# Performance work log

Hardware: AMD Instinct MI355X
Metric: run time of the kernel (lower is better)

The kernel has to match this reference:

```python
import jax, jax.numpy as jnp
import numpy as np

B, H, S, D = 2, 16, 2048, 64
NUM_BUCKETS = 32
MAX_DISTANCE = 256


def setup_inputs() -> dict:
    key = jax.random.key(0)
    kq, kk, kv, kb, kl = jax.random.split(key, 5)
    q = jax.random.normal(kq, (B, H, S, D), dtype=jnp.float32)
    k = jax.random.normal(kk, (B, H, S, D), dtype=jnp.float32)
    v = jax.random.normal(kv, (B, H, S, D), dtype=jnp.float32)
    bias_table = jax.random.normal(kb, (NUM_BUCKETS, H), dtype=jnp.float32)
    event_length = jax.random.randint(kl, (B,), 1, S + 1, dtype=jnp.int64)
    return {"q": q, "k": k, "v": v, "bias_table": bias_table, "event_length": event_length}


def _relative_position_bucket(relative_position):
    # T5-style bucketing exactly as the torch module: n = -rel_pos
    half = NUM_BUCKETS // 2  # 16
    n = -relative_position
    is_small = n < half
    # guard log for the branch not taken (n<=0); where() masks it out
    nf = jnp.maximum(n, 1).astype(jnp.float32)
    val_if_large = half + jnp.minimum(
        jnp.log(nf / half) / np.log(MAX_DISTANCE / half) * (NUM_BUCKETS - half),
        NUM_BUCKETS - 1 - half,
    ).astype(jnp.int32)
    ret = jnp.where(is_small, n, val_if_large)
    return jnp.clip(ret, 0, NUM_BUCKETS - 1)


def _compute_bias(bias_table, seq_len):
    ctx = jnp.arange(seq_len)[:, None]
    mem = jnp.arange(seq_len)[None, :]
    rp_bucket = _relative_position_bucket(mem - ctx)  # (S,S)
    values = bias_table[rp_bucket]                    # (S,S,H)
    return jnp.transpose(values, (2, 0, 1))[None]     # (1,H,S,S)


def reference(q, k, v, bias_table, event_length):
    seq_len = q.shape[2]
    head_dim = q.shape[3]
    # scaled QK^T: (B,H,S,S)
    logits = jnp.einsum("bhsd,bhtd->bhst", q, k) / np.sqrt(head_dim).astype(np.float32)
    logits = logits + _compute_bias(bias_table, seq_len)
    # key-side padding mask from per-event lengths
    mask = jnp.arange(seq_len)[None, None, None, :] < event_length[:, None, None, None]
    logits = jnp.where(mask, logits, jnp.float32(-1e9))
    attn = jax.nn.softmax(logits, axis=-1)
    # dropout p=0.01 omitted (eval-mode deterministic reference)
    return jnp.einsum("bhst,bhtd->bhsd", attn, v)
```

## Files before the change

kernel.cpp:

```cpp
#include <hip/hip_runtime.h>
#include <hip/hip_bf16.h>

#define B_ 2
#define H_ 16
#define S_ 2048
#define D_ 64
#define BQ 128
#define BK 64
#define LDSTR 72
#define LOG2E 1.4426950408889634f
#define FIXM 10.0f

#if __has_builtin(__builtin_amdgcn_exp2f)
#define EXP2F(x) __builtin_amdgcn_exp2f(x)
#else
#define EXP2F(x) __expf((x) * 0.6931471805599453f)
#endif

typedef _Float16 half8 __attribute__((ext_vector_type(8)));
typedef _Float16 half4 __attribute__((ext_vector_type(4)));
typedef __fp16   fp16x2 __attribute__((ext_vector_type(2)));
typedef float floatx4 __attribute__((ext_vector_type(4)));

__global__ __launch_bounds__(256, 2)
void t5_attn_kernel(const float* __restrict__ qg_, const float* __restrict__ kg_,
                    const float* __restrict__ vg_, const float* __restrict__ bt,
                    const int* __restrict__ elen, float* __restrict__ outg_)
{
    __shared__ __align__(16) _Float16 Kl[2][BK][LDSTR];
    __shared__ __align__(16) _Float16 Vt[2][D_][LDSTR];
    __shared__ __align__(16) _Float16 Pl[4][32][LDSTR];
    __shared__ float lut[256];

    const int qblk = blockIdx.x;
    const int h    = blockIdx.y;
    const int b    = blockIdx.z;
    const int tid  = threadIdx.x;
    const int wave = tid >> 6;
    const int lane = tid & 63;
    const int quad = lane >> 4;
    const int t16  = lane & 15;

    {
        int n = tid;
        int bucket;
        if (n < 16) {
            bucket = n;
        } else {
            int vl = (int)(__log2f((float)n * 0.0625f) * 4.0f);
            bucket = 16 + (vl < 15 ? vl : 15);
        }
        lut[n] = bt[bucket * H_ + h] * LOG2E - FIXM;
    }
    const float sh_next = FIXM - bt[h] * LOG2E;
    const float sh_far  = FIXM - bt[31 * H_ + h] * LOG2E;

    const int len = (elen[1] == 0) ? elen[2 * b] : elen[b];
    const int ntiles = (len + BK - 1) >> 6;

    const size_t bh = ((size_t)b * H_ + h) * (size_t)(S_ * D_);
    const float* qg = qg_ + bh;
    const float* kg = kg_ + bh;
    const float* vg = vg_ + bh;
    float*       og = outg_ + bh;

    half8 qf[2][2];
    #pragma unroll
    for (int rg = 0; rg < 2; ++rg) {
        const float qscale = 0.125f * LOG2E;
        const int row = qblk * BQ + wave * 32 + rg * 16 + t16;
        const float* qp = qg + (size_t)row * D_ + quad * 8;
        #pragma unroll
        for (int c = 0; c < 2; ++c) {
            const float4* p = reinterpret_cast<const float4*>(qp + c * 32);
            float4 x0 = p[0], x1 = p[1];
            half8 hv;
            hv[0] = (_Float16)(x0.x * qscale); hv[1] = (_Float16)(x0.y * qscale);
            hv[2] = (_Float16)(x0.z * qscale); hv[3] = (_Float16)(x0.w * qscale);
            hv[4] = (_Float16)(x1.x * qscale); hv[5] = (_Float16)(x1.y * qscale);
            hv[6] = (_Float16)(x1.z * qscale); hv[7] = (_Float16)(x1.w * qscale);
            qf[rg][c] = hv;
        }
    }

    floatx4 zero4 = {0.f, 0.f, 0.f, 0.f};
    floatx4 acc[2][4];
    float l_[2];
    #pragma unroll
    for (int rg = 0; rg < 2; ++rg) {
        #pragma unroll
        for (int nb = 0; nb < 4; ++nb) acc[rg][nb] = zero4;
        l_[rg] = 0.f;
    }

    const int i_lo = qblk * BQ + wave * 32;

    float4 kx[2][2];
    float  vx[16];
    auto prefetch = [&](int kt) {
        #pragma unroll
        for (int it = 0; it < 2; ++it) {
            int idx = tid + it * 256;
            int row = idx >> 3;
            int c8  = (idx & 7) << 3;
            const float4* p = reinterpret_cast<const float4*>(
                kg + ((size_t)(kt * BK + row) * D_ + c8));
            kx[it][0] = p[0];
            kx[it][1] = p[1];
        }
        #pragma unroll
        for (int it = 0; it < 2; ++it) {
            int key8 = kt * BK + wave * 8 + it * 32;
            #pragma unroll
            for (int jj = 0; jj < 8; ++jj)
                vx[it * 8 + jj] = vg[(size_t)(key8 + jj) * D_ + lane];
        }
    };
    auto stage = [&](int buf) {
        #pragma unroll
        for (int it = 0; it < 2; ++it) {
            int idx = tid + it * 256;
            int row = idx >> 3;
            int c8  = (idx & 7) << 3;
            float4 x0 = kx[it][0], x1 = kx[it][1];
            half8 hv;
            hv[0]=(_Float16)x0.x; hv[1]=(_Float16)x0.y; hv[2]=(_Float16)x0.z; hv[3]=(_Float16)x0.w;
            hv[4]=(_Float16)x1.x; hv[5]=(_Float16)x1.y; hv[6]=(_Float16)x1.z; hv[7]=(_Float16)x1.w;
            *reinterpret_cast<half8*>(&Kl[buf][row][c8]) = hv;
        }
        #pragma unroll
        for (int it = 0; it < 2; ++it) {
            int key8 = wave * 8 + it * 32;
            half8 hv;
            #pragma unroll
            for (int jj = 0; jj < 8; ++jj) hv[jj] = (_Float16)vx[it * 8 + jj];
            *reinterpret_cast<half8*>(&Vt[buf][lane][key8]) = hv;
        }
    };

    prefetch(0);
    stage(0);
    __syncthreads();

    for (int kt = 0; kt < ntiles; ++kt) {
        const int cur = kt & 1;
        const bool more = (kt + 1) < ntiles;
        if (more) prefetch(kt + 1);

        floatx4 sa[2][4];
        #pragma unroll
        for (int rg = 0; rg < 2; ++rg)
            #pragma unroll
            for (int nb = 0; nb < 4; ++nb) sa[rg][nb] = zero4;
        #pragma unroll
        for (int kc = 0; kc < 2; ++kc) {
            #pragma unroll
            for (int nb = 0; nb < 4; ++nb) {
                half8 af = *reinterpret_cast<const half8*>(
                    &Kl[cur][nb * 16 + t16][kc * 32 + quad * 8]);
                sa[0][nb] = __builtin_amdgcn_mfma_f32_16x16x32_f16(af, qf[0][kc], sa[0][nb], 0, 0, 0);
                sa[1][nb] = __builtin_amdgcn_mfma_f32_16x16x32_f16(af, qf[1][kc], sa[1][nb], 0, 0, 0);
            }
        }

        const int base = kt * BK;
        if (i_lo + 31 <= base) {
            #pragma unroll
            for (int rg = 0; rg < 2; ++rg)
                #pragma unroll
                for (int nb = 0; nb < 4; ++nb)
                    #pragma unroll
                    for (int r = 0; r < 4; ++r) sa[rg][nb][r] -= sh_next;
        } else if (i_lo >= base + 279) {
            #pragma unroll
            for (int rg = 0; rg < 2; ++rg)
                #pragma unroll
                for (int nb = 0; nb < 4; ++nb)
                    #pragma unroll
                    for (int r = 0; r < 4; ++r) sa[rg][nb][r] -= sh_far;
        } else {
            #pragma unroll
            for (int rg = 0; rg < 2; ++rg) {
                const int d0 = i_lo + rg * 16 + t16 - base - quad * 4;
                #pragma unroll
                for (int nb = 0; nb < 4; ++nb) {
                    #pragma unroll
                    for (int r = 0; r < 4; ++r) {
                        int d = d0 - nb * 16 - r;
                        d = d < 0 ? 0 : (d > 255 ? 255 : d);
                        sa[rg][nb][r] += lut[d];
                    }
                }
            }
        }
        if ((kt == ntiles - 1) && (len & 63)) {
            #pragma unroll
            for (int nb = 0; nb < 4; ++nb) {
                #pragma unroll
                for (int r = 0; r < 4; ++r) {
                    bool valid = (base + nb * 16 + quad * 4 + r) < len;
                    #pragma unroll
                    for (int rg = 0; rg < 2; ++rg)
                        sa[rg][nb][r] = valid ? sa[rg][nb][r] : -1e30f;
                }
            }
        }

        #pragma unroll
        for (int rg = 0; rg < 2; ++rg) {
            float s = 0.f;
            #pragma unroll
            for (int nb = 0; nb < 4; ++nb)
                #pragma unroll
                for (int r = 0; r < 4; ++r) {
                    sa[rg][nb][r] = EXP2F(sa[rg][nb][r]);
                    s += sa[rg][nb][r];
                }
            l_[rg] += s;
        }

        #pragma unroll
        for (int rg = 0; rg < 2; ++rg) {
            #pragma unroll
            for (int nb = 0; nb < 4; ++nb) {
                fp16x2 lo = __builtin_amdgcn_cvt_pkrtz(sa[rg][nb][0], sa[rg][nb][1]);
                fp16x2 hi = __builtin_amdgcn_cvt_pkrtz(sa[rg][nb][2], sa[rg][nb][3]);
                half4 w;
                w[0] = (_Float16)lo[0]; w[1] = (_Float16)lo[1];
                w[2] = (_Float16)hi[0]; w[3] = (_Float16)hi[1];
                *reinterpret_cast<half4*>(
                    &Pl[wave][rg * 16 + t16][nb * 16 + quad * 4]) = w;
            }
        }
        asm volatile("s_waitcnt lgkmcnt(0)" ::: "memory");

        #pragma unroll
        for (int kc = 0; kc < 2; ++kc) {
            half8 a0 = *reinterpret_cast<const half8*>(
                &Pl[wave][t16][kc * 32 + quad * 8]);
            half8 a1 = *reinterpret_cast<const half8*>(
                &Pl[wave][16 + t16][kc * 32 + quad * 8]);
            #pragma unroll
            for (int nb = 0; nb < 4; ++nb) {
                half8 bv = *reinterpret_cast<const half8*>(
                    &Vt[cur][nb * 16 + t16][kc * 32 + quad * 8]);
                acc[0][nb] = __builtin_amdgcn_mfma_f32_16x16x32_f16(a0, bv, acc[0][nb], 0, 0, 0);
                acc[1][nb] = __builtin_amdgcn_mfma_f32_16x16x32_f16(a1, bv, acc[1][nb], 0, 0, 0);
            }
        }

        if (more) stage(cur ^ 1);
        __syncthreads();
    }

    #pragma unroll
    for (int rg = 0; rg < 2; ++rg) {
        float lv = l_[rg];
        lv += __shfl_xor(lv, 16, 64);
        lv += __shfl_xor(lv, 32, 64);
        float inv = 1.f / lv;
        #pragma unroll
        for (int r = 0; r < 4; ++r) {
            int rowloc = quad * 4 + r;
            float invr = __shfl(inv, (lane & 48) | rowloc, 64);
            const int row = qblk * BQ + wave * 32 + rg * 16 + rowloc;
            #pragma unroll
            for (int nb = 0; nb < 4; ++nb)
                og[(size_t)row * D_ + nb * 16 + t16] = acc[rg][nb][r] * invr;
        }
    }
}

extern "C" void kernel_launch(void* const* d_in, const int* in_sizes, int n_in,
                              void* d_out, int out_size, void* d_ws, size_t ws_size,
                              hipStream_t stream) {
    const float* q  = (const float*)d_in[0];
    const float* k  = (const float*)d_in[1];
    const float* v  = (const float*)d_in[2];
    const float* bt = (const float*)d_in[3];
    const int*   el = (const int*)d_in[4];
    float* out = (float*)d_out;
    dim3 grid(S_ / BQ, H_, B_);
    t5_attn_kernel<<<grid, 256, 0, stream>>>(q, k, v, bt, el, out);
}
```

Baseline: 117.6 us.

## Process key tiles in pairs with register-staged fp16 prefetch and interleaved grid

The key loop now handles two 64-key tiles per iteration. Both K and V tiles are loaded from global memory and converted to fp16 in registers ahead of time, then written to LDS between two barriers, and the P staging buffer is widened to hold 128 keys. This halves the number of loop iterations and barrier points and gives the QK^T MFMAs more independent work. The grid becomes 1D with batch and head interleaved in the low bits, which changes block scheduling order and could balance the uneven per-batch sequence lengths. In exchange it uses more registers and LDS, which may lower occupancy. It also wastes a masked half-pair when the tile count is odd and adds an extra barrier per iteration.

```diff
diff --git a/kernel.cpp b/kernel.cpp
--- a/kernel.cpp
+++ b/kernel.cpp
@@ -8,6 +8,7 @@
 #define BQ 128
 #define BK 64
 #define LDSTR 72
+#define PSTR 136
 #define LOG2E 1.4426950408889634f
 #define FIXM 10.0f
 
@@ -29,12 +30,13 @@
 {
     __shared__ __align__(16) _Float16 Kl[2][BK][LDSTR];
     __shared__ __align__(16) _Float16 Vt[2][D_][LDSTR];
-    __shared__ __align__(16) _Float16 Pl[4][32][LDSTR];
+    __shared__ __align__(16) _Float16 Pl[4][32][PSTR];
     __shared__ float lut[256];
 
-    const int qblk = blockIdx.x;
-    const int h    = blockIdx.y;
-    const int b    = blockIdx.z;
+    const int bx   = blockIdx.x;
+    const int b    = bx & 1;
+    const int h    = (bx >> 1) & 15;
+    const int qblk = bx >> 5;
     const int tid  = threadIdx.x;
     const int wave = tid >> 6;
     const int lane = tid & 63;
@@ -57,6 +59,7 @@
 
     const int len = (elen[1] == 0) ? elen[2 * b] : elen[b];
     const int ntiles = (len + BK - 1) >> 6;
+    const int npairs = (ntiles + 1) >> 1;
 
     const size_t bh = ((size_t)b * H_ + h) * (size_t)(S_ * D_);
     const float* qg = qg_ + bh;
@@ -95,162 +98,188 @@
 
     const int i_lo = qblk * BQ + wave * 32;
 
-    float4 kx[2][2];
-    float  vx[16];
-    auto prefetch = [&](int kt) {
-        #pragma unroll
-        for (int it = 0; it < 2; ++it) {
-            int idx = tid + it * 256;
-            int row = idx >> 3;
-            int c8  = (idx & 7) << 3;
-            const float4* p = reinterpret_cast<const float4*>(
-                kg + ((size_t)(kt * BK + row) * D_ + c8));
-            kx[it][0] = p[0];
-            kx[it][1] = p[1];
-        }
-        #pragma unroll
-        for (int it = 0; it < 2; ++it) {
-            int key8 = kt * BK + wave * 8 + it * 32;
-            #pragma unroll
-            for (int jj = 0; jj < 8; ++jj)
-                vx[it * 8 + jj] = vg[(size_t)(key8 + jj) * D_ + lane];
+    half8 kst[2][2];
+    half8 vst[2][2];
+    const int krow = tid >> 3;
+    const int kc8  = (tid & 7) << 3;
+    auto prefetch = [&](int p) {
+        const int pbase = p * 2 * BK;
+        #pragma unroll
+        for (int t = 0; t < 2; ++t) {
+            #pragma unroll
+            for (int it = 0; it < 2; ++it) {
+                int idx = tid + it * 256;
+                int row = idx >> 3, c8 = (idx & 7) << 3;
+                const float4* pp = reinterpret_cast<const float4*>(
+                    kg + ((size_t)(pbase + t * BK + row) * D_ + c8));
+                float4 x0 = pp[0], x1 = pp[1];
+                half8 hv;
+                hv[0]=(_Float16)x0.x; hv[1]=(_Float16)x0.y; hv[2]=(_Float16)x0.z; hv[3]=(_Float16)x0.w;
+                hv[4]=(_Float16)x1.x; hv[5]=(_Float16)x1.y; hv[6]=(_Float16)x1.z; hv[7]=(_Float16)x1.w;
+                kst[t][it] = hv;
+            }
+            #pragma unroll
+            for (int it = 0; it < 2; ++it) {
+                int key8 = pbase + t * BK + wave * 8 + it * 32;
+                half8 vv;
+                #pragma unroll
+                for (int jj = 0; jj < 8; ++jj)
+                    vv[jj] = (_Float16)vg[(size_t)(key8 + jj) * D_ + lane];
+                vst[t][it] = vv;
+            }
         }
     };
-    auto stage = [&](int buf) {
-        #pragma unroll
-        for (int it = 0; it < 2; ++it) {
-            int idx = tid + it * 256;
-            int row = idx >> 3;
-            int c8  = (idx & 7) << 3;
-            float4 x0 = kx[it][0], x1 = kx[it][1];
-            half8 hv;
-            hv[0]=(_Float16)x0.x; hv[1]=(_Float16)x0.y; hv[2]=(_Float16)x0.z; hv[3]=(_Float16)x0.w;
-            hv[4]=(_Float16)x1.x; hv[5]=(_Float16)x1.y; hv[6]=(_Float16)x1.z; hv[7]=(_Float16)x1.w;
-            *reinterpret_cast<half8*>(&Kl[buf][row][c8]) = hv;
-        }
-        #pragma unroll
-        for (int it = 0; it < 2; ++it) {
-            int key8 = wave * 8 + it * 32;
-            half8 hv;
-            #pragma unroll
-            for (int jj = 0; jj < 8; ++jj) hv[jj] = (_Float16)vx[it * 8 + jj];
-            *reinterpret_cast<half8*>(&Vt[buf][lane][key8]) = hv;
+    auto stage = [&]() {
+        #pragma unroll
+        for (int t = 0; t < 2; ++t) {
+            #pragma unroll
+            for (int it = 0; it < 2; ++it) {
+                int idx = tid + it * 256;
+                int row = idx >> 3, c8 = (idx & 7) << 3;
+                *reinterpret_cast<half8*>(&Kl[t][row][c8]) = kst[t][it];
+                *reinterpret_cast<half8*>(&Vt[t][lane][wave * 8 + it * 32]) = vst[t][it];
+            }
         }
     };
 
     prefetch(0);
-    stage(0);
+    stage();
     __syncthreads();
 
-    for (int kt = 0; kt < ntiles; ++kt) {
-        const int cur = kt & 1;
-        const bool more = (kt + 1) < ntiles;
-        if (more) prefetch(kt + 1);
-
-        floatx4 sa[2][4];
-        #pragma unroll
-        for (int rg = 0; rg < 2; ++rg)
-            #pragma unroll
-            for (int nb = 0; nb < 4; ++nb) sa[rg][nb] = zero4;
+    for (int p = 0; p < npairs; ++p) {
+        const bool more = (p + 1) < npairs;
+
+        floatx4 sa[2][2][4];
+        #pragma unroll
+        for (int t = 0; t < 2; ++t)
+            #pragma unroll
+            for (int rg = 0; rg < 2; ++rg)
+                #pragma unroll
+                for (int nb = 0; nb < 4; ++nb) sa[t][rg][nb] = zero4;
         #pragma unroll
         for (int kc = 0; kc < 2; ++kc) {
             #pragma unroll
             for (int nb = 0; nb < 4; ++nb) {
-                half8 af = *reinterpret_cast<const half8*>(
-                    &Kl[cur][nb * 16 + t16][kc * 32 + quad * 8]);
-                sa[0][nb] = __builtin_amdgcn_mfma_f32_16x16x32_f16(af, qf[0][kc], sa[0][nb], 0, 0, 0);
-                sa[1][nb] = __builtin_amdgcn_mfma_f32_16x16x32_f16(af, qf[1][kc], sa[1][nb], 0, 0, 0);
-            }
-        }
-
-        const int base = kt * BK;
-        if (i_lo + 31 <= base) {
-            #pragma unroll
-            for (int rg = 0; rg < 2; ++rg)
-                #pragma unroll
-                for (int nb = 0; nb < 4; ++nb)
-                    #pragma unroll
-                    for (int r = 0; r < 4; ++r) sa[rg][nb][r] -= sh_next;
-        } else if (i_lo >= base + 279) {
-            #pragma unroll
-            for (int rg = 0; rg < 2; ++rg)
-                #pragma unroll
-                for (int nb = 0; nb < 4; ++nb)
-                    #pragma unroll
-                    for (int r = 0; r < 4; ++r) sa[rg][nb][r] -= sh_far;
-        } else {
-            #pragma unroll
-            for (int rg = 0; rg < 2; ++rg) {
-                const int d0 = i_lo + rg * 16 + t16 - base - quad * 4;
-                #pragma unroll
-                for (int nb = 0; nb < 4; ++nb) {
-                    #pragma unroll
-                    for (int r = 0; r < 4; ++r) {
-                        int d = d0 - nb * 16 - r;
-                        d = d < 0 ? 0 : (d > 255 ? 255 : d);
-                        sa[rg][nb][r] += lut[d];
+                half8 af0 = *reinterpret_cast<const half8*>(
+                    &Kl[0][nb * 16 + t16][kc * 32 + quad * 8]);
+                half8 af1 = *reinterpret_cast<const half8*>(
+                    &Kl[1][nb * 16 + t16][kc * 32 + quad * 8]);
+                sa[0][0][nb] = __builtin_amdgcn_mfma_f32_16x16x32_f16(af0, qf[0][kc], sa[0][0][nb], 0, 0, 0);
+                sa[1][0][nb] = __builtin_amdgcn_mfma_f32_16x16x32_f16(af1, qf[0][kc], sa[1][0][nb], 0, 0, 0);
+                sa[0][1][nb] = __builtin_amdgcn_mfma_f32_16x16x32_f16(af0, qf[1][kc], sa[0][1][nb], 0, 0, 0);
+                sa[1][1][nb] = __builtin_amdgcn_mfma_f32_16x16x32_f16(af1, qf[1][kc], sa[1][1][nb], 0, 0, 0);
+            }
+        }
+
+        if (more) prefetch(p + 1);
+
+        #pragma unroll
+        for (int t = 0; t < 2; ++t) {
+            const int kt = 2 * p + t;
+            const int base = kt * BK;
+            if (kt >= ntiles) {
+                #pragma unroll
+                for (int rg = 0; rg < 2; ++rg)
+                    #pragma unroll
+                    for (int nb = 0; nb < 4; ++nb)
+                        #pragma unroll
+                        for (int r = 0; r < 4; ++r) sa[t][rg][nb][r] = -1e30f;
+            } else if (i_lo + 31 <= base) {
+                #pragma unroll
+                for (int rg = 0; rg < 2; ++rg)
+                    #pragma unroll
+                    for (int nb = 0; nb < 4; ++nb)
+                        #pragma unroll
+                        for (int r = 0; r < 4; ++r) sa[t][rg][nb][r] -= sh_next;
+            } else if (i_lo >= base + 279) {
+                #pragma unroll
+                for (int rg = 0; rg < 2; ++rg)
+                    #pragma unroll
+                    for (int nb = 0; nb < 4; ++nb)
+                        #pragma unroll
+                        for (int r = 0; r < 4; ++r) sa[t][rg][nb][r] -= sh_far;
+            } else {
+                #pragma unroll
+                for (int rg = 0; rg < 2; ++rg) {
+                    const int d0 = i_lo + rg * 16 + t16 - base - quad * 4;
+                    #pragma unroll
+                    for (int nb = 0; nb < 4; ++nb) {
+                        #pragma unroll
+                        for (int r = 0; r < 4; ++r) {
+                            int d = d0 - nb * 16 - r;
+                            d = d < 0 ? 0 : (d > 255 ? 255 : d);
+                            sa[t][rg][nb][r] += lut[d];
+                        }
                     }
                 }
             }
-        }
-        if ((kt == ntiles - 1) && (len & 63)) {
-            #pragma unroll
-            for (int nb = 0; nb < 4; ++nb) {
-                #pragma unroll
-                for (int r = 0; r < 4; ++r) {
-                    bool valid = (base + nb * 16 + quad * 4 + r) < len;
-                    #pragma unroll
-                    for (int rg = 0; rg < 2; ++rg)
-                        sa[rg][nb][r] = valid ? sa[rg][nb][r] : -1e30f;
+            if ((kt == ntiles - 1) && (len & 63)) {
+                #pragma unroll
+                for (int nb = 0; nb < 4; ++nb) {
+                    #pragma unroll
+                    for (int r = 0; r < 4; ++r) {
+                        bool valid = (base + nb * 16 + quad * 4 + r) < len;
+                        #pragma unroll
+                        for (int rg = 0; rg < 2; ++rg)
+                            sa[t][rg][nb][r] = valid ? sa[t][rg][nb][r] : -1e30f;
+                    }
                 }
             }
-        }
-
-        #pragma unroll
-        for (int rg = 0; rg < 2; ++rg) {
-            float s = 0.f;
-            #pragma unroll
-            for (int nb = 0; nb < 4; ++nb)
-                #pragma unroll
-                for (int r = 0; r < 4; ++r) {
-                    sa[rg][nb][r] = EXP2F(sa[rg][nb][r]);
-                    s += sa[rg][nb][r];
+            #pragma unroll
+            for (int rg = 0; rg < 2; ++rg) {
+                float s = 0.f;
+                #pragma unroll
+                for (int nb = 0; nb < 4; ++nb)
+                    #pragma unroll
+                    for (int r = 0; r < 4; ++r) {
+                        sa[t][rg][nb][r] = EXP2F(sa[t][rg][nb][r]);
+                        s += sa[t][rg][nb][r];
+                    }
+                l_[rg] += s;
+            }
+        }
+
+        #pragma unroll
+        for (int t = 0; t < 2; ++t) {
+            #pragma unroll
+            for (int rg = 0; rg < 2; ++rg) {
+                #pragma unroll
+                for (int nb = 0; nb < 4; ++nb) {
+                    fp16x2 lo = __builtin_amdgcn_cvt_pkrtz(sa[t][rg][nb][0], sa[t][rg][nb][1]);
+                    fp16x2 hi = __builtin_amdgcn_cvt_pkrtz(sa[t][rg][nb][2], sa[t][rg][nb][3]);
+                    half4 w;
+                    w[0] = (_Float16)lo[0]; w[1] = (_Float16)lo[1];
+                    w[2] = (_Float16)hi[0]; w[3] = (_Float16)hi[1];
+                    *reinterpret_cast<half4*>(
+                        &Pl[wave][rg * 16 + t16][t * 64 + nb * 16 + quad * 4]) = w;
                 }
-            l_[rg] += s;
-        }
-
-        #pragma unroll
-        for (int rg = 0; rg < 2; ++rg) {
-            #pragma unroll
-            for (int nb = 0; nb < 4; ++nb) {
-                fp16x2 lo = __builtin_amdgcn_cvt_pkrtz(sa[rg][nb][0], sa[rg][nb][1]);
-                fp16x2 hi = __builtin_amdgcn_cvt_pkrtz(sa[rg][nb][2], sa[rg][nb][3]);
-                half4 w;
-                w[0] = (_Float16)lo[0]; w[1] = (_Float16)lo[1];
-                w[2] = (_Float16)hi[0]; w[3] = (_Float16)hi[1];
-                *reinterpret_cast<half4*>(
-                    &Pl[wave][rg * 16 + t16][nb * 16 + quad * 4]) = w;
             }
         }
         asm volatile("s_waitcnt lgkmcnt(0)" ::: "memory");
 
         #pragma unroll
-        for (int kc = 0; kc < 2; ++kc) {
-            half8 a0 = *reinterpret_cast<const half8*>(
-                &Pl[wave][t16][kc * 32 + quad * 8]);
-            half8 a1 = *reinterpret_cast<const half8*>(
-                &Pl[wave][16 + t16][kc * 32 + quad * 8]);
-            #pragma unroll
-            for (int nb = 0; nb < 4; ++nb) {
-                half8 bv = *reinterpret_cast<const half8*>(
-                    &Vt[cur][nb * 16 + t16][kc * 32 + quad * 8]);
-                acc[0][nb] = __builtin_amdgcn_mfma_f32_16x16x32_f16(a0, bv, acc[0][nb], 0, 0, 0);
-                acc[1][nb] = __builtin_amdgcn_mfma_f32_16x16x32_f16(a1, bv, acc[1][nb], 0, 0, 0);
-            }
-        }
-
-        if (more) stage(cur ^ 1);
-        __syncthreads();
+        for (int t = 0; t < 2; ++t) {
+            #pragma unroll
+            for (int kc = 0; kc < 2; ++kc) {
+                half8 a0 = *reinterpret_cast<const half8*>(
+                    &Pl[wave][t16][t * 64 + kc * 32 + quad * 8]);
+                half8 a1 = *reinterpret_cast<const half8*>(
+                    &Pl[wave][16 + t16][t * 64 + kc * 32 + quad * 8]);
+                #pragma unroll
+                for (int nb = 0; nb < 4; ++nb) {
+                    half8 bv = *reinterpret_cast<const half8*>(
+                        &Vt[t][nb * 16 + t16][kc * 32 + quad * 8]);
+                    acc[0][nb] = __builtin_amdgcn_mfma_f32_16x16x32_f16(a0, bv, acc[0][nb], 0, 0, 0);
+                    acc[1][nb] = __builtin_amdgcn_mfma_f32_16x16x32_f16(a1, bv, acc[1][nb], 0, 0, 0);
+                }
+            }
+        }
+
+        if (more) {
+            __syncthreads();
+            stage();
+            __syncthreads();
+        }
     }
 
     #pragma unroll
@@ -280,6 +309,5 @@
     const float* bt = (const float*)d_in[3];
     const int*   el = (const int*)d_in[4];
     float* out = (float*)d_out;
-    dim3 grid(S_ / BQ, H_, B_);
-    t5_attn_kernel<<<grid, 256, 0, stream>>>(q, k, v, bt, el, out);
+    t5_attn_kernel<<<dim3((S_ / BQ) * H_ * B_), dim3(256), 0, stream>>>(q, k, v, bt, el, out);
 }
```

Result: slower. 122.5 us (+4.2%).

## Split key tile across two wave teams with 64-row query blocks and LDS reduction

Applied to the files above, without the earlier changes.

Query block size is halved to 64 rows, and the four waves form two teams that each handle half of every 64-key tile for the same 32 query rows. The partial outputs and row sums are combined through LDS at the end. The grid is flattened with batch and head in the low bits, and launch bounds are raised to allow three blocks per CU. This doubles the block count to improve occupancy and load balance across CUs, at the cost of K/V being re-staged for twice as many blocks plus an extra cross-team reduction.

```diff
diff --git a/kernel.cpp b/kernel.cpp
--- a/kernel.cpp
+++ b/kernel.cpp
@@ -5,9 +5,10 @@
 #define H_ 16
 #define S_ 2048
 #define D_ 64
-#define BQ 128
+#define BQ 64
 #define BK 64
 #define LDSTR 72
+#define PSTR 40
 #define LOG2E 1.4426950408889634f
 #define FIXM 10.0f
 
@@ -22,24 +23,28 @@
 typedef __fp16   fp16x2 __attribute__((ext_vector_type(2)));
 typedef float floatx4 __attribute__((ext_vector_type(4)));
 
-__global__ __launch_bounds__(256, 2)
+__global__ __launch_bounds__(256, 3)
 void t5_attn_kernel(const float* __restrict__ qg_, const float* __restrict__ kg_,
                     const float* __restrict__ vg_, const float* __restrict__ bt,
                     const int* __restrict__ elen, float* __restrict__ outg_)
 {
     __shared__ __align__(16) _Float16 Kl[2][BK][LDSTR];
     __shared__ __align__(16) _Float16 Vt[2][D_][LDSTR];
-    __shared__ __align__(16) _Float16 Pl[4][32][LDSTR];
+    __shared__ __align__(16) _Float16 Pp[4][32][PSTR];
     __shared__ float lut[256];
 
-    const int qblk = blockIdx.x;
-    const int h    = blockIdx.y;
-    const int b    = blockIdx.z;
+    const int bx   = blockIdx.x;
+    const int b    = bx & 1;
+    const int h    = (bx >> 1) & 15;
+    const int qblk = bx >> 5;
     const int tid  = threadIdx.x;
     const int wave = tid >> 6;
     const int lane = tid & 63;
     const int quad = lane >> 4;
     const int t16  = lane & 15;
+    const int team = wave >> 1;
+    const int wv   = wave & 1;
+    const int tb   = team * 32;
 
     {
         int n = tid;
@@ -68,7 +73,7 @@
     #pragma unroll
     for (int rg = 0; rg < 2; ++rg) {
         const float qscale = 0.125f * LOG2E;
-        const int row = qblk * BQ + wave * 32 + rg * 16 + t16;
+        const int row = qblk * BQ + wv * 32 + rg * 16 + t16;
         const float* qp = qg + (size_t)row * D_ + quad * 8;
         #pragma unroll
         for (int c = 0; c < 2; ++c) {
@@ -93,7 +98,7 @@
         l_[rg] = 0.f;
     }
 
-    const int i_lo = qblk * BQ + wave * 32;
+    const int i_lo = qblk * BQ + wv * 32;
 
     float4 kx[2][2];
     float  vx[16];
@@ -131,10 +136,10 @@
         #pragma unroll
         for (int it = 0; it < 2; ++it) {
             int key8 = wave * 8 + it * 32;
-            half8 hv;
-            #pragma unroll
-            for (int jj = 0; jj < 8; ++jj) hv[jj] = (_Float16)vx[it * 8 + jj];
-            *reinterpret_cast<half8*>(&Vt[buf][lane][key8]) = hv;
+            half8 vv;
+            #pragma unroll
+            for (int jj = 0; jj < 8; ++jj) vv[jj] = (_Float16)vx[it * 8 + jj];
+            *reinterpret_cast<half8*>(&Vt[buf][lane][key8]) = vv;
         }
     };
 
@@ -147,35 +152,35 @@
         const bool more = (kt + 1) < ntiles;
         if (more) prefetch(kt + 1);
 
-        floatx4 sa[2][4];
+        floatx4 sa[2][2];
         #pragma unroll
         for (int rg = 0; rg < 2; ++rg)
             #pragma unroll
-            for (int nb = 0; nb < 4; ++nb) sa[rg][nb] = zero4;
+            for (int nb = 0; nb < 2; ++nb) sa[rg][nb] = zero4;
         #pragma unroll
         for (int kc = 0; kc < 2; ++kc) {
             #pragma unroll
-            for (int nb = 0; nb < 4; ++nb) {
+            for (int nb = 0; nb < 2; ++nb) {
                 half8 af = *reinterpret_cast<const half8*>(
-                    &Kl[cur][nb * 16 + t16][kc * 32 + quad * 8]);
+                    &Kl[cur][tb + nb * 16 + t16][kc * 32 + quad * 8]);
                 sa[0][nb] = __builtin_amdgcn_mfma_f32_16x16x32_f16(af, qf[0][kc], sa[0][nb], 0, 0, 0);
                 sa[1][nb] = __builtin_amdgcn_mfma_f32_16x16x32_f16(af, qf[1][kc], sa[1][nb], 0, 0, 0);
             }
         }
 
-        const int base = kt * BK;
+        const int base = kt * BK + tb;
         if (i_lo + 31 <= base) {
             #pragma unroll
             for (int rg = 0; rg < 2; ++rg)
                 #pragma unroll
-                for (int nb = 0; nb < 4; ++nb)
+                for (int nb = 0; nb < 2; ++nb)
                     #pragma unroll
                     for (int r = 0; r < 4; ++r) sa[rg][nb][r] -= sh_next;
-        } else if (i_lo >= base + 279) {
+        } else if (i_lo >= base + 247) {
             #pragma unroll
             for (int rg = 0; rg < 2; ++rg)
                 #pragma unroll
-                for (int nb = 0; nb < 4; ++nb)
+                for (int nb = 0; nb < 2; ++nb)
                     #pragma unroll
                     for (int r = 0; r < 4; ++r) sa[rg][nb][r] -= sh_far;
         } else {
@@ -183,7 +188,7 @@
             for (int rg = 0; rg < 2; ++rg) {
                 const int d0 = i_lo + rg * 16 + t16 - base - quad * 4;
                 #pragma unroll
-                for (int nb = 0; nb < 4; ++nb) {
+                for (int nb = 0; nb < 2; ++nb) {
                     #pragma unroll
                     for (int r = 0; r < 4; ++r) {
                         int d = d0 - nb * 16 - r;
@@ -195,7 +200,7 @@
         }
         if ((kt == ntiles - 1) && (len & 63)) {
             #pragma unroll
-            for (int nb = 0; nb < 4; ++nb) {
+            for (int nb = 0; nb < 2; ++nb) {
                 #pragma unroll
                 for (int r = 0; r < 4; ++r) {
                     bool valid = (base + nb * 16 + quad * 4 + r) < len;
@@ -210,7 +215,7 @@
         for (int rg = 0; rg < 2; ++rg) {
             float s = 0.f;
             #pragma unroll
-            for (int nb = 0; nb < 4; ++nb)
+            for (int nb = 0; nb < 2; ++nb)
                 #pragma unroll
                 for (int r = 0; r < 4; ++r) {
                     sa[rg][nb][r] = EXP2F(sa[rg][nb][r]);
@@ -222,28 +227,25 @@
         #pragma unroll
         for (int rg = 0; rg < 2; ++rg) {
             #pragma unroll
-            for (int nb = 0; nb < 4; ++nb) {
+            for (int nb = 0; nb < 2; ++nb) {
                 fp16x2 lo = __builtin_amdgcn_cvt_pkrtz(sa[rg][nb][0], sa[rg][nb][1]);
                 fp16x2 hi = __builtin_amdgcn_cvt_pkrtz(sa[rg][nb][2], sa[rg][nb][3]);
                 half4 w;
                 w[0] = (_Float16)lo[0]; w[1] = (_Float16)lo[1];
                 w[2] = (_Float16)hi[0]; w[3] = (_Float16)hi[1];
                 *reinterpret_cast<half4*>(
-                    &Pl[wave][rg * 16 + t16][nb * 16 + quad * 4]) = w;
+                    &Pp[wave][rg * 16 + t16][nb * 16 + quad * 4]) = w;
             }
         }
         asm volatile("s_waitcnt lgkmcnt(0)" ::: "memory");
 
-        #pragma unroll
-        for (int kc = 0; kc < 2; ++kc) {
-            half8 a0 = *reinterpret_cast<const half8*>(
-                &Pl[wave][t16][kc * 32 + quad * 8]);
-            half8 a1 = *reinterpret_cast<const half8*>(
-                &Pl[wave][16 + t16][kc * 32 + quad * 8]);
+        {
+            half8 a0 = *reinterpret_cast<const half8*>(&Pp[wave][t16][quad * 8]);
+            half8 a1 = *reinterpret_cast<const half8*>(&Pp[wave][16 + t16][quad * 8]);
             #pragma unroll
             for (int nb = 0; nb < 4; ++nb) {
                 half8 bv = *reinterpret_cast<const half8*>(
-                    &Vt[cur][nb * 16 + t16][kc * 32 + quad * 8]);
+                    &Vt[cur][nb * 16 + t16][tb + quad * 8]);
                 acc[0][nb] = __builtin_amdgcn_mfma_f32_16x16x32_f16(a0, bv, acc[0][nb], 0, 0, 0);
                 acc[1][nb] = __builtin_amdgcn_mfma_f32_16x16x32_f16(a1, bv, acc[1][nb], 0, 0, 0);
             }
@@ -253,20 +255,45 @@
         __syncthreads();
     }
 
+    float lv[2];
     #pragma unroll
     for (int rg = 0; rg < 2; ++rg) {
-        float lv = l_[rg];
-        lv += __shfl_xor(lv, 16, 64);
-        lv += __shfl_xor(lv, 32, 64);
-        float inv = 1.f / lv;
-        #pragma unroll
-        for (int r = 0; r < 4; ++r) {
-            int rowloc = quad * 4 + r;
-            float invr = __shfl(inv, (lane & 48) | rowloc, 64);
-            const int row = qblk * BQ + wave * 32 + rg * 16 + rowloc;
+        lv[rg] = l_[rg];
+        lv[rg] += __shfl_xor(lv[rg], 16, 64);
+        lv[rg] += __shfl_xor(lv[rg], 32, 64);
+    }
+    float* cb = reinterpret_cast<float*>(&Kl[0][0][0]);
+    if (team == 1) {
+        #pragma unroll
+        for (int rg = 0; rg < 2; ++rg) {
             #pragma unroll
             for (int nb = 0; nb < 4; ++nb)
-                og[(size_t)row * D_ + nb * 16 + t16] = acc[rg][nb][r] * invr;
+                #pragma unroll
+                for (int r = 0; r < 4; ++r)
+                    cb[wv * 2048 + (rg * 16 + quad * 4 + r) * 64 + nb * 16 + t16]
+                        = acc[rg][nb][r];
+            if (quad == 0)
+                cb[4096 + wv * 32 + rg * 16 + t16] = lv[rg];
+        }
+    }
+    __syncthreads();
+    if (team == 0) {
+        #pragma unroll
+        for (int rg = 0; rg < 2; ++rg) {
+            float ltot = lv[rg] + cb[4096 + wv * 32 + rg * 16 + t16];
+            float inv = 1.f / ltot;
+            #pragma unroll
+            for (int r = 0; r < 4; ++r) {
+                int rowloc = quad * 4 + r;
+                float invr = __shfl(inv, (lane & 48) | rowloc, 64);
+                const int row = qblk * BQ + wv * 32 + rg * 16 + rowloc;
+                #pragma unroll
+                for (int nb = 0; nb < 4; ++nb) {
+                    float o = acc[rg][nb][r]
+                            + cb[wv * 2048 + (rg * 16 + rowloc) * 64 + nb * 16 + t16];
+                    og[(size_t)row * D_ + nb * 16 + t16] = o * invr;
+                }
+            }
         }
     }
 }
@@ -280,6 +307,5 @@
     const float* bt = (const float*)d_in[3];
     const int*   el = (const int*)d_in[4];
     float* out = (float*)d_out;
-    dim3 grid(S_ / BQ, H_, B_);
-    t5_attn_kernel<<<grid, 256, 0, stream>>>(q, k, v, bt, el, out);
+    t5_attn_kernel<<<dim3((S_ / BQ) * H_ * B_), dim3(256), 0, stream>>>(q, k, v, bt, el, out);
 }
```

After: 132.4 us. +12.7%, slower.
